# Performance work log

Hardware: AMD Instinct MI355X
Metric: run time of the kernel (lower is better)

Reference implementation:

```python
import jax, jax.numpy as jnp
import numpy as np
from jax import lax

B, T, HW = 8, 32, 128
D, NH, DEPTH, DFF = 384, 6, 6, 1536
PR = PC = 4
P = PR * PC
EPS = 1e-5


def _ln(x, g, b):
    mu = x.mean(-1, keepdims=True)
    v = ((x - mu) ** 2).mean(-1, keepdims=True)
    return (x - mu) / jnp.sqrt(v + EPS) * g + b


def _conv2d(x, w, s, p):
    return lax.conv_general_dilated(x, w, (s, s), [(p, p), (p, p)],
                                    dimension_numbers=('NCHW', 'OIHW', 'NCHW'))


def _bn(x, g, b, m, v):
    inv = g / jnp.sqrt(v + EPS)
    return x * inv[:, None, None] + (b - m * inv)[:, None, None]


def _gelu(x):
    return jax.nn.gelu(x, approximate=False)


def _forward(frames, conv1_w, bn1_g, bn1_b, bn1_m, bn1_v,
             conv2_w, bn2_g, bn2_b, bn2_m, bn2_v,
             conv3_w, bn3_g, bn3_b, bn3_m, bn3_v, proj_w,
             dw_w, dw_b, pw_w, pw_b, tnorm_g, tnorm_b,
             frame_pos, patch_pos, cls_token, cls_pos,
             qkv_w, qkv_b, out_w, out_b, ln1_g, ln1_b, ln2_g, ln2_b,
             ffn_w1, ffn_b1, ffn_w2, ffn_b2,
             head_ln_g, head_ln_b, head_w1, head_b1, head_w2, head_b2):
    b, t = frames.shape[0], frames.shape[1]
    # ---- FrameEncoder (eval-mode BN) ----
    x = frames.reshape(b * t, 1, HW, HW)
    x = _gelu(_bn(_conv2d(x, conv1_w, 2, 2), bn1_g, bn1_b, bn1_m, bn1_v))
    x = _gelu(_bn(_conv2d(x, conv2_w, 2, 1), bn2_g, bn2_b, bn2_m, bn2_v))
    x = _gelu(_bn(_conv2d(x, conv3_w, 2, 1), bn3_g, bn3_b, bn3_m, bn3_v))
    n, c, hh, ww = x.shape
    # adaptive avg pool (16,16)->(4,4) is an exact 4x4 mean pool
    x = x.reshape(n, c, PR, hh // PR, PC, ww // PC).mean(axis=(3, 5))
    x = jnp.einsum('oc,nchw->nohw', proj_w[:, :, 0, 0], x)  # 1x1 conv proj
    tokens = x.reshape(n, D, P).transpose(0, 2, 1).reshape(b, t, P, D)
    # ---- TemporalConvBlock (per-patch sequences) ----
    tc = tokens.transpose(0, 2, 1, 3).reshape(b * P, t, D)
    out = tc.transpose(0, 2, 1)  # [N, D, t]
    for i, dil in enumerate((1, 2)):
        pad = dil * (3 - 1) // 2
        h = lax.conv_general_dilated(out, dw_w[i], (1,), [(pad, pad)],
                                     rhs_dilation=(dil,), feature_group_count=D,
                                     dimension_numbers=('NCH', 'OIH', 'NCH'))
        h = _gelu(h + dw_b[i][None, :, None])
        h = jnp.einsum('oi,nit->not', pw_w[i], h) + pw_b[i][None, :, None]
        out = h + out
    out = out.transpose(0, 2, 1)
    tc = _ln(out + tc, tnorm_g, tnorm_b)
    tokens = tc.reshape(b, P, t, D).transpose(0, 2, 1, 3)
    # ---- positional + cls ----
    fp = frame_pos[:t].transpose(1, 0, 2)[:, :, None, :]  # [1,t,1,D]
    pp = patch_pos[:, None, :, :]                          # [1,1,P,D]
    tok = (tokens + fp + pp).reshape(b, t * P, D)
    cls = cls_token + cls_pos
    tok = jnp.concatenate([jnp.broadcast_to(cls, (b, 1, D)), tok], axis=1)
    S = t * P + 1
    # ---- block-structured additive mask (faithful to _build_causal_mask) ----
    ids = jnp.repeat(jnp.arange(t), P)
    neg = jnp.finfo(jnp.float32).min
    base = jnp.where(ids[None, :] < ids[:, None], neg, 0.0)
    mask = jnp.zeros((S, S), jnp.float32).at[1:, 1:].set(base).at[1:, 0].set(neg)
    # ---- pre-norm transformer encoder ----
    hd = D // NH
    scale = 1.0 / jnp.sqrt(jnp.float32(hd))
    x = tok
    for i in range(DEPTH):
        h = _ln(x, ln1_g[i], ln1_b[i])
        qkv = h @ qkv_w[i].T + qkv_b[i]
        q, k, v = jnp.split(qkv, 3, axis=-1)
        q = q.reshape(b, S, NH, hd).transpose(0, 2, 1, 3)
        k = k.reshape(b, S, NH, hd).transpose(0, 2, 1, 3)
        v = v.reshape(b, S, NH, hd).transpose(0, 2, 1, 3)
        scores = jnp.einsum('bhqd,bhkd->bhqk', q, k) * scale + mask
        a = jax.nn.softmax(scores, axis=-1)
        o = jnp.einsum('bhqk,bhkd->bhqd', a, v).transpose(0, 2, 1, 3).reshape(b, S, D)
        x = x + (o @ out_w[i].T + out_b[i])
        h2 = _ln(x, ln2_g[i], ln2_b[i])
        x = x + _gelu(h2 @ ffn_w1[i].T + ffn_b1[i]) @ ffn_w2[i].T + ffn_b2[i]
    # ---- coord head ----
    pooled = x[:, 0]
    h = _ln(pooled, head_ln_g, head_ln_b)
    h = _gelu(h @ head_w1.T + head_b1)
    coords = jax.nn.sigmoid(h @ head_w2.T + head_b2)
    return coords


def setup_inputs():
    ks = iter(jax.random.split(jax.random.key(0), 64))

    def r(shape, s):
        return jax.random.normal(next(ks), shape, jnp.float32) * s

    inp = {}
    inp['frames'] = jax.random.normal(next(ks), (B, T, 1, HW, HW), jnp.float32)
    inp['conv1_w'] = r((32, 1, 5, 5), 0.2)
    inp['bn1_g'] = jnp.ones(32); inp['bn1_b'] = jnp.zeros(32)
    inp['bn1_m'] = r((32,), 0.1)
    inp['bn1_v'] = jax.random.uniform(next(ks), (32,), jnp.float32, 0.5, 1.5)
    inp['conv2_w'] = r((64, 32, 3, 3), 0.1)
    inp['bn2_g'] = jnp.ones(64); inp['bn2_b'] = jnp.zeros(64)
    inp['bn2_m'] = r((64,), 0.1)
    inp['bn2_v'] = jax.random.uniform(next(ks), (64,), jnp.float32, 0.5, 1.5)
    inp['conv3_w'] = r((128, 64, 3, 3), 0.07)
    inp['bn3_g'] = jnp.ones(128); inp['bn3_b'] = jnp.zeros(128)
    inp['bn3_m'] = r((128,), 0.1)
    inp['bn3_v'] = jax.random.uniform(next(ks), (128,), jnp.float32, 0.5, 1.5)
    inp['proj_w'] = r((D, 128, 1, 1), 0.08)
    inp['dw_w'] = r((2, D, 1, 3), 0.3)
    inp['dw_b'] = jnp.zeros((2, D))
    inp['pw_w'] = r((2, D, D), 0.05)
    inp['pw_b'] = jnp.zeros((2, D))
    inp['tnorm_g'] = jnp.ones(D); inp['tnorm_b'] = jnp.zeros(D)
    inp['frame_pos'] = r((T, 1, D), 0.02)
    inp['patch_pos'] = r((1, P, D), 0.02)
    inp['cls_token'] = jnp.zeros((1, 1, D))
    inp['cls_pos'] = r((1, 1, D), 0.02)
    inp['qkv_w'] = r((DEPTH, 3 * D, D), 0.02)
    inp['qkv_b'] = jnp.zeros((DEPTH, 3 * D))
    inp['out_w'] = r((DEPTH, D, D), 0.02)
    inp['out_b'] = jnp.zeros((DEPTH, D))
    inp['ln1_g'] = jnp.ones((DEPTH, D)); inp['ln1_b'] = jnp.zeros((DEPTH, D))
    inp['ln2_g'] = jnp.ones((DEPTH, D)); inp['ln2_b'] = jnp.zeros((DEPTH, D))
    inp['ffn_w1'] = r((DEPTH, DFF, D), 0.02)
    inp['ffn_b1'] = jnp.zeros((DEPTH, DFF))
    inp['ffn_w2'] = r((DEPTH, D, DFF), 0.02)
    inp['ffn_b2'] = jnp.zeros((DEPTH, D))
    inp['head_ln_g'] = jnp.ones(D); inp['head_ln_b'] = jnp.zeros(D)
    inp['head_w1'] = r((D, D), 0.02); inp['head_b1'] = jnp.zeros(D)
    inp['head_w2'] = r((2, D), 0.02); inp['head_b2'] = jnp.zeros(2)
    return inp


def reference(frames, conv1_w, bn1_g, bn1_b, bn1_m, bn1_v,
              conv2_w, bn2_g, bn2_b, bn2_m, bn2_v,
              conv3_w, bn3_g, bn3_b, bn3_m, bn3_v, proj_w,
              dw_w, dw_b, pw_w, pw_b, tnorm_g, tnorm_b,
              frame_pos, patch_pos, cls_token, cls_pos,
              qkv_w, qkv_b, out_w, out_b, ln1_g, ln1_b, ln2_g, ln2_b,
              ffn_w1, ffn_b1, ffn_w2, ffn_b2,
              head_ln_g, head_ln_b, head_w1, head_b1, head_w2, head_b2):
    return _forward(frames, conv1_w, bn1_g, bn1_b, bn1_m, bn1_v,
                    conv2_w, bn2_g, bn2_b, bn2_m, bn2_v,
                    conv3_w, bn3_g, bn3_b, bn3_m, bn3_v, proj_w,
                    dw_w, dw_b, pw_w, pw_b, tnorm_g, tnorm_b,
                    frame_pos, patch_pos, cls_token, cls_pos,
                    qkv_w, qkv_b, out_w, out_b, ln1_g, ln1_b, ln2_g, ln2_b,
                    ffn_w1, ffn_b1, ffn_w2, ffn_b2,
                    head_ln_g, head_ln_b, head_w1, head_b1, head_w2, head_b2)
```

## Files before the change

### kernel.cpp

```cpp
#include <hip/hip_runtime.h>
#include <hip/hip_fp16.h>
#include <cstddef>

#define EPSV 1e-5f

typedef _Float16 f16;
typedef _Float16 f16x8 __attribute__((ext_vector_type(8)));
typedef float f32x4v __attribute__((ext_vector_type(4)));

__device__ __forceinline__ float gelu_f(float x) {
    return 0.5f * x * (1.0f + erff(x * 0.7071067811865476f));
}

__device__ __forceinline__ float gelu_fast(float x) {
    float y = 0.7978845608f * (x + 0.044715f * x * x * x);
    y = fminf(fmaxf(y, -10.f), 10.f);
    float e = __expf(2.f * y);
    float t = (e - 1.f) / (e + 1.f);
    return 0.5f * x * (1.f + t);
}

__global__ __launch_bounds__(256) void cvt_all_kernel(
    const float* __restrict__ p0, const float* __restrict__ p1,
    const float* __restrict__ p2, const float* __restrict__ p3,
    const float* __restrict__ p4, const float* __restrict__ p5,
    f16* __restrict__ dst)
{
    const int n = 10960896;
    for (int i = blockIdx.x * 256 + threadIdx.x; i < n; i += gridDim.x * 256) {
        const float* s; int off;
        if      (i <   49152) { s = p0; off = i; }
        else if (i <  344064) { s = p1; off = i -   49152; }
        else if (i < 2998272) { s = p2; off = i -  344064; }
        else if (i < 3883008) { s = p3; off = i - 2998272; }
        else if (i < 7421952) { s = p4; off = i - 3883008; }
        else                  { s = p5; off = i - 7421952; }
        dst[i] = (f16)s[off];
    }
}

__global__ __launch_bounds__(256) void conv_w_reorder_kernel(
    const float* __restrict__ w, f16* __restrict__ out, int CO, int CI)
{
    int n = CO * CI * 9;
    for (int i = blockIdx.x * 256 + threadIdx.x; i < n; i += gridDim.x * 256) {
        int t = i % 9; int r = i / 9;
        int ci = r % CI; int co = r / CI;
        out[(size_t)co * CI * 9 + t * CI + ci] = (f16)w[i];
    }
}

__global__ __launch_bounds__(256) void conv1_wave_kernel(
    const float* __restrict__ in, const float* __restrict__ w,
    const float* __restrict__ g, const float* __restrict__ bt,
    const float* __restrict__ mn, const float* __restrict__ vr,
    f16* __restrict__ out)
{
    __shared__ float inp[35][37];
    int bid = blockIdx.x;
    int n = bid >> 4; int tile = bid & 15;
    int ty0 = (tile >> 2) * 16, tx0 = (tile & 3) * 16;
    int t = threadIdx.x;
    const float* ip = in + (size_t)n * 16384;
    for (int e = t; e < 35 * 36; e += 256) {
        int r = e / 36, c = e - r * 36;
        int iy = ty0 * 2 - 2 + r, ix = tx0 * 2 - 2 + c;
        inp[r][c] = ((unsigned)iy < 128u && (unsigned)ix < 128u) ? ip[iy * 128 + ix] : 0.f;
    }
    __syncthreads();
    int wv = __builtin_amdgcn_readfirstlane(t >> 6);
    int lane = t & 63;
    int cobase = wv * 8;
    float sc[8], be[8];
    #pragma unroll
    for (int c = 0; c < 8; c++) {
        int co = cobase + c;
        float iv = g[co] * rsqrtf(vr[co] + EPSV);
        sc[c] = iv; be[c] = bt[co] - mn[co] * iv;
    }
    #pragma unroll
    for (int pix = 0; pix < 4; pix++) {
        int p = pix * 64 + lane;
        int py = p >> 4, px = p & 15;
        float r0[25];
        #pragma unroll
        for (int ky = 0; ky < 5; ky++)
            #pragma unroll
            for (int kx = 0; kx < 5; kx++)
                r0[ky * 5 + kx] = inp[2 * py + ky][2 * px + kx];
        f16 o[8];
        #pragma unroll
        for (int c = 0; c < 8; c++) {
            const float* wp = w + (cobase + c) * 25;
            float acc = 0.f;
            #pragma unroll
            for (int k = 0; k < 25; k++) acc += wp[k] * r0[k];
            o[c] = (f16)gelu_fast(acc * sc[c] + be[c]);
        }
        size_t ob = (((size_t)n * 64 + ty0 + py) * 64 + tx0 + px) * 32 + cobase;
        *(uint4*)(out + ob) = *(uint4*)o;
    }
}

template<int CI, int HI, int CO>
__global__ __launch_bounds__(256) void convg_kernel(
    const f16* __restrict__ in, const f16* __restrict__ wr_,
    const float* __restrict__ g, const float* __restrict__ bt,
    const float* __restrict__ mn, const float* __restrict__ vr,
    f16* __restrict__ out)
{
    constexpr int HO = HI / 2;
    constexpr int HOB = (HO == 32) ? 5 : 4;
    constexpr int K = 9 * CI;
    __shared__ __align__(16) f16 As[64 * 40];
    __shared__ __align__(16) f16 Bs[64 * 40];
    int tid = threadIdx.x;
    int bm = blockIdx.x * 64;
    int bn = blockIdx.y * 64;
    int lrow = tid >> 2, lseg = tid & 3;
    int w = tid >> 6, lane = tid & 63;
    int wr = (w >> 1) * 32, wc = (w & 1) * 32;
    int l15 = lane & 15, l4 = lane >> 4;
    int gp = bm + lrow;
    int pn = gp >> (2 * HOB);
    int prem = gp & ((1 << (2 * HOB)) - 1);
    int oy = prem >> HOB, ox = prem & (HO - 1);

    f32x4v zero = {0.f, 0.f, 0.f, 0.f};
    f32x4v acc[2][2];
    acc[0][0] = zero; acc[0][1] = zero; acc[1][0] = zero; acc[1][1] = zero;

    auto loadTile = [&](int k0, uint4& av, uint4& bv) {
        int tap = k0 / CI;
        int cio = k0 - tap * CI;
        int ky = tap / 3, kx = tap - ky * 3;
        int iy = oy * 2 - 1 + ky, ix = ox * 2 - 1 + kx;
        av = make_uint4(0u, 0u, 0u, 0u);
        if ((unsigned)iy < (unsigned)HI && (unsigned)ix < (unsigned)HI)
            av = *(const uint4*)(in + (((size_t)(pn * HI + iy)) * HI + ix) * CI + cio + lseg * 8);
        bv = *(const uint4*)(wr_ + (size_t)(bn + lrow) * K + k0 + lseg * 8);
    };

    uint4 ra, rb;
    loadTile(0, ra, rb);
    for (int k0 = 0; k0 < K; k0 += 32) {
        __syncthreads();
        *(uint4*)(&As[lrow * 40 + lseg * 8]) = ra;
        *(uint4*)(&Bs[lrow * 40 + lseg * 8]) = rb;
        if (k0 + 32 < K) loadTile(k0 + 32, ra, rb);
        __syncthreads();
        f16x8 a0 = *(const f16x8*)(&As[(wr + l15) * 40 + l4 * 8]);
        f16x8 a1 = *(const f16x8*)(&As[(wr + 16 + l15) * 40 + l4 * 8]);
        f16x8 b0 = *(const f16x8*)(&Bs[(wc + l15) * 40 + l4 * 8]);
        f16x8 b1 = *(const f16x8*)(&Bs[(wc + 16 + l15) * 40 + l4 * 8]);
        acc[0][0] = __builtin_amdgcn_mfma_f32_16x16x32_f16(a0, b0, acc[0][0], 0, 0, 0);
        acc[0][1] = __builtin_amdgcn_mfma_f32_16x16x32_f16(a0, b1, acc[0][1], 0, 0, 0);
        acc[1][0] = __builtin_amdgcn_mfma_f32_16x16x32_f16(a1, b0, acc[1][0], 0, 0, 0);
        acc[1][1] = __builtin_amdgcn_mfma_f32_16x16x32_f16(a1, b1, acc[1][1], 0, 0, 0);
    }
    float inv[2], beta[2];
    #pragma unroll
    for (int ni = 0; ni < 2; ni++) {
        int col = bn + wc + ni * 16 + l15;
        float iv = g[col] * rsqrtf(vr[col] + EPSV);
        inv[ni] = iv; beta[ni] = bt[col] - mn[col] * iv;
    }
    #pragma unroll
    for (int mi = 0; mi < 2; mi++) {
        #pragma unroll
        for (int q = 0; q < 4; q++) {
            int pixel = bm + wr + mi * 16 + l4 * 4 + q;
            #pragma unroll
            for (int ni = 0; ni < 2; ni++) {
                int col = bn + wc + ni * 16 + l15;
                float v = acc[mi][ni][q] * inv[ni] + beta[ni];
                out[(size_t)pixel * CO + col] = (f16)gelu_fast(v);
            }
        }
    }
}

__global__ __launch_bounds__(256) void poolh_kernel(
    const f16* __restrict__ in, f16* __restrict__ out, int NC)
{
    int idx = blockIdx.x * 256 + threadIdx.x;
    if (idx >= NC * 16 * 16) return;
    int cc = idx & 15; int npl = idx >> 4;
    int c0 = cc * 8;
    int n = npl >> 4; int p = npl & 15;
    int ph = p >> 2, pw = p & 3;
    const f16* base = in + (((size_t)(n * 16 + ph * 4)) * 16 + pw * 4) * 128 + c0;
    float s[8] = {};
    #pragma unroll
    for (int dy = 0; dy < 4; dy++)
        #pragma unroll
        for (int dx = 0; dx < 4; dx++) {
            f16x8 v = *(const f16x8*)(base + (dy * 16 + dx) * 128);
            #pragma unroll
            for (int u = 0; u < 8; u++) s[u] += (float)v[u];
        }
    f16* op = out + (size_t)npl * 128 + c0;
    #pragma unroll
    for (int u = 0; u < 8; u++) op[u] = (f16)(s[u] * 0.0625f);
}

template<int OUTF16, int ACT, int VTRANS>
__global__ __launch_bounds__(256) void gemm_k64_kernel(
    const f16* __restrict__ A, const f16* __restrict__ B,
    const float* __restrict__ bias, const float* __restrict__ res,
    void* __restrict__ Cv, f16* __restrict__ vT, int M, int N, int K, int nrow)
{
    __shared__ __align__(16) f16 As[64 * 72];
    __shared__ __align__(16) f16 Bs[64 * 72];
    int nb = gridDim.x;
    int q = nb >> 3, r = nb & 7;
    int xcd = blockIdx.x & 7, pos = blockIdx.x >> 3;
    int logical = (xcd < r ? xcd * (q + 1) : r * (q + 1) + (xcd - r) * q) + pos;
    int brow = logical % nrow, bcol = logical / nrow;
    int bm = brow * 64, bn = bcol * 64;

    int tid = threadIdx.x;
    int lrow = tid >> 2, lseg = (tid & 3) * 16;
    int w = tid >> 6, lane = tid & 63;
    int wr = (w >> 1) * 32, wc = (w & 1) * 32;
    int l15 = lane & 15, l4 = lane >> 4;
    f32x4v zero = {0.f, 0.f, 0.f, 0.f};
    f32x4v acc[2][2];
    acc[0][0] = zero; acc[0][1] = zero; acc[1][0] = zero; acc[1][1] = zero;

    int arow = bm + lrow;
    bool aok = (arow < M);
    const f16* ap = A + (size_t)arow * K + lseg;
    const f16* bp = B + (size_t)(bn + lrow) * K + lseg;

    uint4 ra0 = make_uint4(0u,0u,0u,0u), ra1 = ra0, rb0, rb1;
    if (aok) { ra0 = *(const uint4*)(ap); ra1 = *(const uint4*)(ap + 8); }
    rb0 = *(const uint4*)(bp); rb1 = *(const uint4*)(bp + 8);

    int nt = K >> 6;
    for (int t = 0; t < nt; t++) {
        __syncthreads();
        *(uint4*)(&As[lrow * 72 + lseg])     = ra0;
        *(uint4*)(&As[lrow * 72 + lseg + 8]) = ra1;
        *(uint4*)(&Bs[lrow * 72 + lseg])     = rb0;
        *(uint4*)(&Bs[lrow * 72 + lseg + 8]) = rb1;
        if (t + 1 < nt) {
            int k0 = (t + 1) << 6;
            if (aok) { ra0 = *(const uint4*)(ap + k0); ra1 = *(const uint4*)(ap + k0 + 8); }
            rb0 = *(const uint4*)(bp + k0); rb1 = *(const uint4*)(bp + k0 + 8);
        }
        __syncthreads();
        #pragma unroll
        for (int s = 0; s < 2; s++) {
            f16x8 a0 = *(const f16x8*)(&As[(wr + l15) * 72 + s * 32 + l4 * 8]);
            f16x8 a1 = *(const f16x8*)(&As[(wr + 16 + l15) * 72 + s * 32 + l4 * 8]);
            f16x8 b0 = *(const f16x8*)(&Bs[(wc + l15) * 72 + s * 32 + l4 * 8]);
            f16x8 b1 = *(const f16x8*)(&Bs[(wc + 16 + l15) * 72 + s * 32 + l4 * 8]);
            acc[0][0] = __builtin_amdgcn_mfma_f32_16x16x32_f16(a0, b0, acc[0][0], 0, 0, 0);
            acc[0][1] = __builtin_amdgcn_mfma_f32_16x16x32_f16(a0, b1, acc[0][1], 0, 0, 0);
            acc[1][0] = __builtin_amdgcn_mfma_f32_16x16x32_f16(a1, b0, acc[1][0], 0, 0, 0);
            acc[1][1] = __builtin_amdgcn_mfma_f32_16x16x32_f16(a1, b1, acc[1][1], 0, 0, 0);
        }
    }

    if (VTRANS && bn >= 768) {
        __syncthreads();
        f16* tile = As;
        #pragma unroll
        for (int mi = 0; mi < 2; mi++)
            #pragma unroll
            for (int qq = 0; qq < 4; qq++) {
                int rl = wr + mi * 16 + l4 * 4 + qq;
                #pragma unroll
                for (int ni = 0; ni < 2; ni++) {
                    int dl = wc + ni * 16 + l15;
                    float v = acc[mi][ni][qq] + bias[bn + dl];
                    tile[dl * 66 + rl] = (f16)v;
                }
            }
        __syncthreads();
        int h = (bn - 768) >> 6;
        int j = tid & 63, dbase = tid >> 6;
        int trow = bm + j;
        if (trow < M) {
            int b = trow / 513;
            int jj = trow - b * 513;
            f16* vb = vT + ((size_t)(b * 6 + h) * 64) * 576 + jj;
            #pragma unroll
            for (int it = 0; it < 16; it++) {
                int d = dbase * 16 + it;
                vb[(size_t)d * 576] = tile[d * 66 + j];
            }
        }
        return;
    }
    #pragma unroll
    for (int mi = 0; mi < 2; mi++) {
        #pragma unroll
        for (int qq = 0; qq < 4; qq++) {
            int row = bm + wr + mi * 16 + l4 * 4 + qq;
            if (row >= M) continue;
            #pragma unroll
            for (int ni = 0; ni < 2; ni++) {
                int col = bn + wc + ni * 16 + l15;
                float v = acc[mi][ni][qq];
                if (bias) v += bias[col];
                if (ACT == 1) v = gelu_fast(v);
                if (res) v += res[(size_t)row * N + col];
                if (OUTF16) ((f16*)Cv)[(size_t)row * N + col] = (f16)v;
                else ((float*)Cv)[(size_t)row * N + col] = v;
            }
        }
    }
}

__global__ __launch_bounds__(256) void tok2tc_kernel(
    const float* __restrict__ in, float* __restrict__ out)
{
    int idx = blockIdx.x * 256 + threadIdx.x;
    if (idx >= 8 * 32 * 16 * 384) return;
    int d = idx % 384; int t2 = idx / 384;
    int p = t2 & 15; t2 >>= 4;
    int t = t2 & 31; int b = t2 >> 5;
    out[(((size_t)(b * 16 + p) * 32 + t) * 384) + d] = in[idx];
}

__global__ __launch_bounds__(256) void dwconv_kernel(
    const float* __restrict__ in, const float* __restrict__ w,
    const float* __restrict__ bias, f16* __restrict__ out, int dil)
{
    int idx = blockIdx.x * 256 + threadIdx.x;
    if (idx >= 128 * 32 * 384) return;
    int d = idx % 384; int t = (idx / 384) & 31; int s = idx / (384 * 32);
    const float* ip = in + (size_t)s * 32 * 384 + d;
    float acc = bias[d];
    #pragma unroll
    for (int k = 0; k < 3; k++) {
        int tt = t + (k - 1) * dil;
        if ((unsigned)tt < 32u) acc += w[d * 3 + k] * ip[tt * 384];
    }
    out[idx] = (f16)gelu_fast(acc);
}

__global__ __launch_bounds__(256) void ln_wave_kernel(
    const float* __restrict__ in,
    const float* __restrict__ g, const float* __restrict__ b,
    f16* __restrict__ out, int rows)
{
    int w = threadIdx.x >> 6, lane = threadIdx.x & 63;
    int row = blockIdx.x * 4 + w;
    if (row >= rows) return;
    const float* ip = in + (size_t)row * 384;
    float x[6]; float s = 0.f, s2 = 0.f;
    #pragma unroll
    for (int k = 0; k < 6; k++) {
        float v = ip[lane + 64 * k];
        x[k] = v; s += v; s2 += v * v;
    }
    #pragma unroll
    for (int off = 1; off < 64; off <<= 1) {
        s += __shfl_xor(s, off); s2 += __shfl_xor(s2, off);
    }
    float mu = s * (1.f / 384.f);
    float var = s2 * (1.f / 384.f) - mu * mu;
    float rs = rsqrtf(var + EPSV);
    #pragma unroll
    for (int k = 0; k < 6; k++) {
        int c = lane + 64 * k;
        out[(size_t)row * 384 + c] = (f16)((x[k] - mu) * rs * g[c] + b[c]);
    }
}

__global__ __launch_bounds__(128) void build_x_kernel(
    const float* __restrict__ mix, const float* __restrict__ tc,
    const float* __restrict__ tg, const float* __restrict__ tb,
    const float* __restrict__ fpos, const float* __restrict__ ppos,
    float* __restrict__ x)
{
    int row = blockIdx.x;
    int t = row & 31; int bp = row >> 5;
    int p = bp & 15; int b = bp >> 4;
    int tid = threadIdx.x;
    const float* ip = mix + (size_t)row * 384;
    const float* ip2 = tc + (size_t)row * 384;
    __shared__ float red[128], red2[128];
    float v[3]; float s = 0.f, s2 = 0.f;
    #pragma unroll
    for (int j = 0; j < 3; j++) {
        float val = ip[tid + 128 * j] + ip2[tid + 128 * j];
        v[j] = val; s += val; s2 += val * val;
    }
    red[tid] = s; red2[tid] = s2; __syncthreads();
    for (int off = 64; off >= 1; off >>= 1) {
        if (tid < off) { red[tid] += red[tid + off]; red2[tid] += red2[tid + off]; }
        __syncthreads();
    }
    float mu = red[0] * (1.f / 384.f);
    float var = red2[0] * (1.f / 384.f) - mu * mu;
    float rs = rsqrtf(var + EPSV);
    size_t xbase = ((size_t)b * 513 + 1 + t * 16 + p) * 384;
    #pragma unroll
    for (int j = 0; j < 3; j++) {
        int c = tid + 128 * j;
        float y = (v[j] - mu) * rs * tg[c] + tb[c] + fpos[t * 384 + c] + ppos[p * 384 + c];
        x[xbase + c] = y;
    }
}

__global__ __launch_bounds__(256) void cls_kernel(
    const float* __restrict__ ct, const float* __restrict__ cp, float* __restrict__ x)
{
    int idx = blockIdx.x * 256 + threadIdx.x;
    if (idx >= 8 * 384) return;
    int c = idx % 384; int b = idx / 384;
    x[(size_t)b * 513 * 384 + c] = ct[c] + cp[c];
}

__global__ __launch_bounds__(256) void fattn_split_kernel(
    const f16* __restrict__ qkv, const f16* __restrict__ vT,
    float* __restrict__ Op, float* __restrict__ ml)
{
    __shared__ __align__(16) f16 Pl[4][16][72];
    int qt = blockIdx.x;
    int bh = blockIdx.y; int h = bh % 6; int b = bh / 6;
    int third = blockIdx.z;
    int tid = threadIdx.x;
    int w = tid >> 6, lane = tid & 63;
    int l15 = lane & 15, g = lane >> 4;
    int q0w = qt * 64 + w * 16;
    if (q0w > 512) return;
    const size_t RS = 1152;
    const f16* qbase = qkv + (size_t)b * 513 * RS + h * 64;
    const f16* kbase = qbase + 384;
    const f16* vtb = vT + (size_t)bh * 64 * 576;

    f16x8 qf[2];
    {
        int qrow = q0w + l15; if (qrow > 512) qrow = 512;
        const f16* qp = qbase + (size_t)qrow * RS + g * 8;
        qf[0] = *(const f16x8*)(qp);
        qf[1] = *(const f16x8*)(qp + 32);
    }

    f32x4v zero = {0.f, 0.f, 0.f, 0.f};
    f32x4v O[4]; float m[4], l[4];
    #pragma unroll
    for (int i = 0; i < 4; i++) { O[i] = zero; m[i] = -INFINITY; l[i] = 0.f; }

    int jt0 = 0;
    if (q0w > 0) { int fmin = (q0w - 1) >> 4; jt0 = (fmin * 16 + 1) >> 6; }

    int jrow[4];
    #pragma unroll
    for (int jf = 0; jf < 4; jf++) jrow[jf] = jf * 16 + l15;

    auto loadK = [&](int j0, f16x8* kr) {
        #pragma unroll
        for (int s = 0; s < 2; s++)
            #pragma unroll
            for (int jf = 0; jf < 4; jf++) {
                int j = j0 + jrow[jf]; if (j > 512) j = 512;
                kr[s * 4 + jf] = *(const f16x8*)(kbase + (size_t)j * RS + s * 32 + g * 8);
            }
    };

    int jt = jt0 + third;
    f16x8 kreg[8];
    if (jt < 9) loadK(jt * 64, kreg);

    for (; jt < 9; jt += 3) {
        int j0 = jt * 64;
        f16x8 vreg[8];
        #pragma unroll
        for (int s = 0; s < 2; s++)
            #pragma unroll
            for (int df = 0; df < 4; df++)
                vreg[s * 4 + df] = *(const f16x8*)(vtb + (size_t)(df * 16 + l15) * 576 + j0 + s * 32 + g * 8);
        f32x4v S[4];
        #pragma unroll
        for (int jf = 0; jf < 4; jf++) S[jf] = zero;
        #pragma unroll
        for (int s = 0; s < 2; s++)
            #pragma unroll
            for (int jf = 0; jf < 4; jf++)
                S[jf] = __builtin_amdgcn_mfma_f32_16x16x32_f16(qf[s], kreg[s * 4 + jf], S[jf], 0, 0, 0);
        f16x8 knext[8];
        if (jt + 3 < 9) loadK((jt + 3) * 64, knext);
        float pj[4][4];
        #pragma unroll
        for (int r = 0; r < 4; r++) {
            int qi = q0w + 4 * g + r;
            int fi = (qi == 0) ? -1 : ((qi - 1) >> 4);
            float mx = -INFINITY;
            #pragma unroll
            for (int jf = 0; jf < 4; jf++) {
                int j = j0 + jrow[jf];
                bool valid = (qi < 513) && (j < 513) &&
                             !((qi != 0) && ((j == 0) || (((j - 1) >> 4) < fi)));
                float sv = valid ? S[jf][r] * 0.125f : -INFINITY;
                pj[jf][r] = sv;
                mx = fmaxf(mx, sv);
            }
            mx = fmaxf(mx, __shfl_xor(mx, 1));
            mx = fmaxf(mx, __shfl_xor(mx, 2));
            mx = fmaxf(mx, __shfl_xor(mx, 4));
            mx = fmaxf(mx, __shfl_xor(mx, 8));
            float mn = fmaxf(m[r], mx);
            float alpha = (m[r] == -INFINITY) ? 0.f : __expf(m[r] - mn);
            float ls = 0.f;
            #pragma unroll
            for (int jf = 0; jf < 4; jf++) {
                float p = (pj[jf][r] == -INFINITY) ? 0.f : __expf(pj[jf][r] - mn);
                pj[jf][r] = p; ls += p;
            }
            ls += __shfl_xor(ls, 1); ls += __shfl_xor(ls, 2);
            ls += __shfl_xor(ls, 4); ls += __shfl_xor(ls, 8);
            l[r] = alpha * l[r] + ls;
            m[r] = mn;
            #pragma unroll
            for (int df = 0; df < 4; df++) O[df][r] *= alpha;
        }
        #pragma unroll
        for (int jf = 0; jf < 4; jf++)
            #pragma unroll
            for (int r = 0; r < 4; r++)
                Pl[w][4 * g + r][jf * 16 + l15] = (f16)pj[jf][r];
        #pragma unroll
        for (int s = 0; s < 2; s++) {
            f16x8 pf = *(const f16x8*)(&Pl[w][l15][s * 32 + g * 8]);
            #pragma unroll
            for (int df = 0; df < 4; df++)
                O[df] = __builtin_amdgcn_mfma_f32_16x16x32_f16(pf, vreg[s * 4 + df], O[df], 0, 0, 0);
        }
        #pragma unroll
        for (int i = 0; i < 8; i++) kreg[i] = knext[i];
    }

    int rowbase = third * 24624 + bh * 513;
    #pragma unroll
    for (int r = 0; r < 4; r++) {
        int qi = q0w + 4 * g + r;
        if (qi > 512) continue;
        size_t ro = (size_t)(rowbase + qi);
        #pragma unroll
        for (int df = 0; df < 4; df++)
            Op[ro * 64 + df * 16 + l15] = O[df][r];
        if (l15 == 0) {
            ml[ro * 2 + 0] = m[r];
            ml[ro * 2 + 1] = l[r];
        }
    }
}

__global__ __launch_bounds__(256) void attn_combine_kernel(
    const float* __restrict__ Op, const float* __restrict__ ml,
    f16* __restrict__ ob)
{
    int row = blockIdx.x * 4 + (threadIdx.x >> 6);
    if (row >= 24624) return;
    int lane = threadIdx.x & 63;
    int bh = row / 513, qi = row - bh * 513;
    int b = bh / 6, h = bh - b * 6;
    float mv[3], lv[3], mm = -INFINITY;
    #pragma unroll
    for (int s = 0; s < 3; s++) {
        mv[s] = ml[((size_t)s * 24624 + row) * 2];
        lv[s] = ml[((size_t)s * 24624 + row) * 2 + 1];
        mm = fmaxf(mm, mv[s]);
    }
    float onum = 0.f, lden = 0.f;
    #pragma unroll
    for (int s = 0; s < 3; s++) {
        float a = (mv[s] == -INFINITY) ? 0.f : __expf(mv[s] - mm);
        lden += lv[s] * a;
        onum += Op[((size_t)s * 24624 + row) * 64 + lane] * a;
    }
    ob[((size_t)(b * 513 + qi)) * 384 + h * 64 + lane] = (f16)(onum / lden);
}

__global__ __launch_bounds__(384) void head_kernel(
    const float* __restrict__ x, const float* __restrict__ lg, const float* __restrict__ lb,
    const float* __restrict__ w1, const float* __restrict__ b1,
    const float* __restrict__ w2, const float* __restrict__ b2,
    float* __restrict__ out)
{
    int b = blockIdx.x; int t = threadIdx.x;
    __shared__ float hs[384], h1[384];
    __shared__ float rs[6], rs2[6];
    const float* xp = x + (size_t)b * 513 * 384;
    float v = xp[t];
    float s = v, s2 = v * v;
    #pragma unroll
    for (int off = 32; off >= 1; off >>= 1) {
        s += __shfl_down(s, off); s2 += __shfl_down(s2, off);
    }
    if ((t & 63) == 0) { rs[t >> 6] = s; rs2[t >> 6] = s2; }
    __syncthreads();
    float S = 0.f, S2 = 0.f;
    #pragma unroll
    for (int i = 0; i < 6; i++) { S += rs[i]; S2 += rs2[i]; }
    float mu = S * (1.f / 384.f);
    float var = S2 * (1.f / 384.f) - mu * mu;
    float rstd = rsqrtf(var + EPSV);
    hs[t] = (v - mu) * rstd * lg[t] + lb[t];
    __syncthreads();
    const float* wr = w1 + (size_t)t * 384;
    float acc = b1[t];
    for (int c = 0; c < 384; c += 4) {
        float4 w4 = *reinterpret_cast<const float4*>(wr + c);
        acc += w4.x * hs[c] + w4.y * hs[c + 1] + w4.z * hs[c + 2] + w4.w * hs[c + 3];
    }
    h1[t] = gelu_f(acc);
    __syncthreads();
    float p0 = h1[t] * w2[t], p1 = h1[t] * w2[384 + t];
    #pragma unroll
    for (int off = 32; off >= 1; off >>= 1) {
        p0 += __shfl_down(p0, off); p1 += __shfl_down(p1, off);
    }
    if ((t & 63) == 0) { rs[t >> 6] = p0; rs2[t >> 6] = p1; }
    __syncthreads();
    if (t == 0) {
        float a0 = b2[0], a1 = b2[1];
        #pragma unroll
        for (int i = 0; i < 6; i++) { a0 += rs[i]; a1 += rs2[i]; }
        out[b * 2 + 0] = 1.f / (1.f + expf(-a0));
        out[b * 2 + 1] = 1.f / (1.f + expf(-a1));
    }
}

static inline int cdiv(int a, int b) { return (a + b - 1) / b; }

extern "C" void kernel_launch(void* const* d_in, const int* in_sizes, int n_in,
                              void* d_out, int out_size, void* d_ws, size_t ws_size,
                              hipStream_t stream)
{
    const float* frames  = (const float*)d_in[0];
    const float* conv1_w = (const float*)d_in[1];
    const float* bn1_g = (const float*)d_in[2]; const float* bn1_b = (const float*)d_in[3];
    const float* bn1_m = (const float*)d_in[4]; const float* bn1_v = (const float*)d_in[5];
    const float* conv2_w = (const float*)d_in[6];
    const float* bn2_g = (const float*)d_in[7]; const float* bn2_b = (const float*)d_in[8];
    const float* bn2_m = (const float*)d_in[9]; const float* bn2_v = (const float*)d_in[10];
    const float* conv3_w = (const float*)d_in[11];
    const float* bn3_g = (const float*)d_in[12]; const float* bn3_b = (const float*)d_in[13];
    const float* bn3_m = (const float*)d_in[14]; const float* bn3_v = (const float*)d_in[15];
    const float* proj_w = (const float*)d_in[16];
    const float* dw_w = (const float*)d_in[17]; const float* dw_b = (const float*)d_in[18];
    const float* pw_w = (const float*)d_in[19]; const float* pw_b = (const float*)d_in[20];
    const float* tnorm_g = (const float*)d_in[21]; const float* tnorm_b = (const float*)d_in[22];
    const float* frame_pos = (const float*)d_in[23];
    const float* patch_pos = (const float*)d_in[24];
    const float* cls_token = (const float*)d_in[25];
    const float* cls_pos = (const float*)d_in[26];
    const float* qkv_w = (const float*)d_in[27]; const float* qkv_b = (const float*)d_in[28];
    const float* out_w = (const float*)d_in[29]; const float* out_b = (const float*)d_in[30];
    const float* ln1_g = (const float*)d_in[31]; const float* ln1_b = (const float*)d_in[32];
    const float* ln2_g = (const float*)d_in[33]; const float* ln2_b = (const float*)d_in[34];
    const float* ffn_w1 = (const float*)d_in[35]; const float* ffn_b1 = (const float*)d_in[36];
    const float* ffn_w2 = (const float*)d_in[37]; const float* ffn_b2 = (const float*)d_in[38];
    const float* head_ln_g = (const float*)d_in[39]; const float* head_ln_b = (const float*)d_in[40];
    const float* head_w1 = (const float*)d_in[41]; const float* head_b1 = (const float*)d_in[42];
    const float* head_w2 = (const float*)d_in[43]; const float* head_b2 = (const float*)d_in[44];
    (void)in_sizes; (void)n_in; (void)out_size; (void)ws_size;

    char* base = (char*)d_ws;
    size_t off = 0;
    auto alloc = [&](size_t bytes) { void* p = base + off; off = (off + bytes + 255) & ~(size_t)255; return p; };

    f16* wtotal = (f16*)alloc((size_t)10960896 * 2);
    f16* projw16 = wtotal;
    f16* pw16    = wtotal + 49152;
    f16* qkvw16  = wtotal + 344064;
    f16* outw16  = wtotal + 2998272;
    f16* f1w16   = wtotal + 3883008;
    f16* f2w16   = wtotal + 7421952;
    f16* c2w16   = (f16*)alloc((size_t)64 * 288 * 2);
    f16* c3w16   = (f16*)alloc((size_t)128 * 576 * 2);
    float* tokens = (float*)alloc((size_t)4096 * 384 * 4);
    f16* pooled   = (f16*)alloc((size_t)4096 * 128 * 2);

    size_t ustart = off;
    f16* c1h = (f16*)alloc((size_t)256 * 64 * 64 * 32 * 2);
    f16* c2h = (f16*)alloc((size_t)256 * 32 * 32 * 64 * 2);
    f16* c3h = (f16*)alloc((size_t)256 * 16 * 16 * 128 * 2);
    size_t uend_stem = off;
    off = ustart;
    float* tc = (float*)alloc((size_t)4096 * 384 * 4);
    float* mA = (float*)alloc((size_t)4096 * 384 * 4);
    float* mB = (float*)alloc((size_t)4096 * 384 * 4);
    f16*   mh = (f16*)alloc((size_t)4096 * 384 * 2);
    float* xb   = (float*)alloc((size_t)8 * 513 * 384 * 4);
    f16*   hb   = (f16*)alloc((size_t)8 * 513 * 384 * 2);
    f16*   qkvb = (f16*)alloc((size_t)8 * 513 * 1152 * 2);
    f16*   vTb  = (f16*)alloc((size_t)48 * 64 * 576 * 2);
    f16*   ob   = (f16*)alloc((size_t)8 * 513 * 384 * 2);
    f16*   ffb  = (f16*)alloc((size_t)8 * 513 * 1536 * 2);
    float* Opart = (float*)alloc((size_t)3 * 24624 * 64 * 4);
    float* mlpart = (float*)alloc((size_t)3 * 24624 * 2 * 4);
    if (off < uend_stem) off = uend_stem;

    cvt_all_kernel<<<4096, 256, 0, stream>>>(
        proj_w, pw_w, qkv_w, out_w, ffn_w1, ffn_w2, wtotal);
    conv_w_reorder_kernel<<<cdiv(64 * 288, 256), 256, 0, stream>>>(conv2_w, c2w16, 64, 32);
    conv_w_reorder_kernel<<<cdiv(128 * 576, 256), 256, 0, stream>>>(conv3_w, c3w16, 128, 64);

    conv1_wave_kernel<<<256 * 16, 256, 0, stream>>>(
        frames, conv1_w, bn1_g, bn1_b, bn1_m, bn1_v, c1h);
    convg_kernel<32, 64, 64><<<dim3(4096, 1), 256, 0, stream>>>(
        c1h, c2w16, bn2_g, bn2_b, bn2_m, bn2_v, c2h);
    convg_kernel<64, 32, 128><<<dim3(1024, 2), 256, 0, stream>>>(
        c2h, c3w16, bn3_g, bn3_b, bn3_m, bn3_v, c3h);
    poolh_kernel<<<256, 256, 0, stream>>>(c3h, pooled, 256);
    gemm_k64_kernel<0, 0, 0><<<384, 256, 0, stream>>>(
        pooled, projw16, nullptr, nullptr, tokens, nullptr, 4096, 384, 128, 64);

    tok2tc_kernel<<<cdiv(8 * 32 * 16 * 384, 256), 256, 0, stream>>>(tokens, tc);
    dwconv_kernel<<<cdiv(128 * 32 * 384, 256), 256, 0, stream>>>(
        tc, dw_w, dw_b, mh, 1);
    gemm_k64_kernel<0, 0, 0><<<384, 256, 0, stream>>>(
        mh, pw16, pw_b, tc, mA, nullptr, 4096, 384, 384, 64);
    dwconv_kernel<<<cdiv(128 * 32 * 384, 256), 256, 0, stream>>>(
        mA, dw_w + 384 * 3, dw_b + 384, mh, 2);
    gemm_k64_kernel<0, 0, 0><<<384, 256, 0, stream>>>(
        mh, pw16 + 384 * 384, pw_b + 384, mA, mB, nullptr, 4096, 384, 384, 64);

    build_x_kernel<<<128 * 32, 128, 0, stream>>>(
        mB, tc, tnorm_g, tnorm_b, frame_pos, patch_pos, xb);
    cls_kernel<<<cdiv(8 * 384, 256), 256, 0, stream>>>(cls_token, cls_pos, xb);

    const int M = 8 * 513;
    const int NR = cdiv(M, 64);
    for (int l = 0; l < 6; l++) {
        ln_wave_kernel<<<cdiv(M, 4), 256, 0, stream>>>(xb,
            ln1_g + (size_t)l * 384, ln1_b + (size_t)l * 384, hb, M);
        gemm_k64_kernel<1, 0, 1><<<NR * 18, 256, 0, stream>>>(
            hb, qkvw16 + (size_t)l * 1152 * 384, qkv_b + (size_t)l * 1152,
            nullptr, qkvb, vTb, M, 1152, 384, NR);
        fattn_split_kernel<<<dim3(9, 48, 3), 256, 0, stream>>>(qkvb, vTb, Opart, mlpart);
        attn_combine_kernel<<<cdiv(24624, 4), 256, 0, stream>>>(Opart, mlpart, ob);
        gemm_k64_kernel<0, 0, 0><<<NR * 6, 256, 0, stream>>>(
            ob, outw16 + (size_t)l * 384 * 384, out_b + (size_t)l * 384,
            xb, xb, nullptr, M, 384, 384, NR);
        ln_wave_kernel<<<cdiv(M, 4), 256, 0, stream>>>(xb,
            ln2_g + (size_t)l * 384, ln2_b + (size_t)l * 384, hb, M);
        gemm_k64_kernel<1, 1, 0><<<NR * 24, 256, 0, stream>>>(
            hb, f1w16 + (size_t)l * 1536 * 384, ffn_b1 + (size_t)l * 1536,
            nullptr, ffb, nullptr, M, 1536, 384, NR);
        gemm_k64_kernel<0, 0, 0><<<NR * 6, 256, 0, stream>>>(
            ffb, f2w16 + (size_t)l * 384 * 1536, ffn_b2 + (size_t)l * 384,
            xb, xb, nullptr, M, 384, 1536, NR);
    }

    head_kernel<<<8, 384, 0, stream>>>(
        xb, head_ln_g, head_ln_b, head_w1, head_b1, head_w2, head_b2, (float*)d_out);
}
```

Measured before the change: 869.6 us.

## Use MFMA for conv1, wider-N tile for FFN1 GEMM, fp16 attention partials

Conv1 now runs as a small MFMA GEMM. It uses fp16 input patches in shared memory and BN-scaled fp16 weights prepared by a new prep kernel, replacing the scalar fp32 FMA loop. The FFN1 GEMM gets a dedicated 64x128 tile kernel with an XCD-aware block remap, which halves the block count and raises per-block reuse of the A tile. Split-attention partial outputs are stored as fp16 instead of fp32 to cut the memory traffic between the attention and combine kernels. The costs are reduced precision in conv1 inputs and in the attention partials, and less parallelism in FFN1.

```diff
diff --git a/kernel.cpp b/kernel.cpp
--- a/kernel.cpp
+++ b/kernel.cpp
@@ -50,13 +50,25 @@
     }
 }
 
-__global__ __launch_bounds__(256) void conv1_wave_kernel(
-    const float* __restrict__ in, const float* __restrict__ w,
-    const float* __restrict__ g, const float* __restrict__ bt,
-    const float* __restrict__ mn, const float* __restrict__ vr,
+__global__ __launch_bounds__(256) void conv1_w_prep_kernel(
+    const float* __restrict__ w, const float* __restrict__ g,
+    const float* __restrict__ vr, f16* __restrict__ wB)
+{
+    int i = blockIdx.x * 256 + threadIdx.x;
+    if (i >= 1024) return;
+    int co = i >> 5, k = i & 31;
+    float inv = g[co] * rsqrtf(vr[co] + EPSV);
+    wB[i] = (f16)((k < 25) ? w[co * 25 + k] * inv : 0.f);
+}
+
+__global__ __launch_bounds__(256) void conv1_mfma_kernel(
+    const float* __restrict__ in, const f16* __restrict__ wB,
+    const float* __restrict__ bt, const float* __restrict__ mn,
+    const float* __restrict__ g, const float* __restrict__ vr,
     f16* __restrict__ out)
 {
-    __shared__ float inp[35][37];
+    __shared__ __align__(16) f16 inpH[35 * 36 + 8];
+    __shared__ __align__(16) f16 Bs[32 * 32];
     int bid = blockIdx.x;
     int n = bid >> 4; int tile = bid & 15;
     int ty0 = (tile >> 2) * 16, tx0 = (tile & 3) * 16;
@@ -65,40 +77,61 @@
     for (int e = t; e < 35 * 36; e += 256) {
         int r = e / 36, c = e - r * 36;
         int iy = ty0 * 2 - 2 + r, ix = tx0 * 2 - 2 + c;
-        inp[r][c] = ((unsigned)iy < 128u && (unsigned)ix < 128u) ? ip[iy * 128 + ix] : 0.f;
+        float v = ((unsigned)iy < 128u && (unsigned)ix < 128u && c < 35) ? ip[iy * 128 + ix] : 0.f;
+        inpH[e] = (f16)v;
+    }
+    if (t < 128) {
+        int row = t >> 2, seg = (t & 3) * 8;
+        *(uint4*)(&Bs[row * 32 + seg]) = *(const uint4*)(wB + row * 32 + seg);
     }
     __syncthreads();
-    int wv = __builtin_amdgcn_readfirstlane(t >> 6);
-    int lane = t & 63;
-    int cobase = wv * 8;
-    float sc[8], be[8];
-    #pragma unroll
-    for (int c = 0; c < 8; c++) {
-        int co = cobase + c;
-        float iv = g[co] * rsqrtf(vr[co] + EPSV);
-        sc[c] = iv; be[c] = bt[co] - mn[co] * iv;
-    }
-    #pragma unroll
-    for (int pix = 0; pix < 4; pix++) {
-        int p = pix * 64 + lane;
-        int py = p >> 4, px = p & 15;
-        float r0[25];
-        #pragma unroll
-        for (int ky = 0; ky < 5; ky++)
-            #pragma unroll
-            for (int kx = 0; kx < 5; kx++)
-                r0[ky * 5 + kx] = inp[2 * py + ky][2 * px + kx];
-        f16 o[8];
-        #pragma unroll
-        for (int c = 0; c < 8; c++) {
-            const float* wp = w + (cobase + c) * 25;
-            float acc = 0.f;
-            #pragma unroll
-            for (int k = 0; k < 25; k++) acc += wp[k] * r0[k];
-            o[c] = (f16)gelu_fast(acc * sc[c] + be[c]);
-        }
-        size_t ob = (((size_t)n * 64 + ty0 + py) * 64 + tx0 + px) * 32 + cobase;
-        *(uint4*)(out + ob) = *(uint4*)o;
+    int w = t >> 6, lane = t & 63;
+    int l15 = lane & 15, gq = lane >> 4;
+    f16x8 afr[4];
+    #pragma unroll
+    for (int i = 0; i < 4; i++) {
+        int mt = 4 * w + i;
+        f16 tmp[8];
+        #pragma unroll
+        for (int e = 0; e < 8; e++) {
+            int kk = 8 * gq + e; if (kk > 24) kk = 24;
+            int ky = kk / 5, kx = kk - ky * 5;
+            tmp[e] = inpH[(2 * mt + ky) * 36 + 2 * l15 + kx];
+        }
+        afr[i] = *(f16x8*)tmp;
+    }
+    f16x8 bfr[2];
+    bfr[0] = *(const f16x8*)(&Bs[l15 * 32 + 8 * gq]);
+    bfr[1] = *(const f16x8*)(&Bs[(16 + l15) * 32 + 8 * gq]);
+    f32x4v zero = {0.f, 0.f, 0.f, 0.f};
+    f32x4v acc[4][2];
+    #pragma unroll
+    for (int i = 0; i < 4; i++) { acc[i][0] = zero; acc[i][1] = zero; }
+    #pragma unroll
+    for (int i = 0; i < 4; i++) {
+        acc[i][0] = __builtin_amdgcn_mfma_f32_16x16x32_f16(afr[i], bfr[0], acc[i][0], 0, 0, 0);
+        acc[i][1] = __builtin_amdgcn_mfma_f32_16x16x32_f16(afr[i], bfr[1], acc[i][1], 0, 0, 0);
+    }
+    float beta[2];
+    #pragma unroll
+    for (int nt = 0; nt < 2; nt++) {
+        int co = nt * 16 + l15;
+        float inv = g[co] * rsqrtf(vr[co] + EPSV);
+        beta[nt] = bt[co] - mn[co] * inv;
+    }
+    #pragma unroll
+    for (int i = 0; i < 4; i++) {
+        int y = ty0 + 4 * w + i;
+        #pragma unroll
+        for (int q = 0; q < 4; q++) {
+            int x = tx0 + 4 * gq + q;
+            size_t ob = (((size_t)n * 64 + y) * 64 + x) * 32;
+            #pragma unroll
+            for (int nt = 0; nt < 2; nt++) {
+                int co = nt * 16 + l15;
+                out[ob + co] = (f16)gelu_fast(acc[i][nt][q] + beta[nt]);
+            }
+        }
     }
 }
 
@@ -314,6 +347,92 @@
     }
 }
 
+template<int ACT>
+__global__ __launch_bounds__(256) void gemm_kn128_kernel(
+    const f16* __restrict__ A, const f16* __restrict__ B,
+    const float* __restrict__ bias, f16* __restrict__ C,
+    int M, int N, int K, int nrow)
+{
+    __shared__ __align__(16) f16 As[64 * 72];
+    __shared__ __align__(16) f16 Bs[128 * 72];
+    int nb = gridDim.x;
+    int q = nb >> 3, r = nb & 7;
+    int xcd = blockIdx.x & 7, pos = blockIdx.x >> 3;
+    int logical = (xcd < r ? xcd * (q + 1) : r * (q + 1) + (xcd - r) * q) + pos;
+    int brow = logical % nrow, bcol = logical / nrow;
+    int bm = brow * 64, bn = bcol * 128;
+
+    int tid = threadIdx.x;
+    int w = tid >> 6, lane = tid & 63;
+    int wr = (w >> 1) * 32, wc = (w & 1) * 64;
+    int l15 = lane & 15, l4 = lane >> 4;
+    int alrow = tid >> 2, alseg = (tid & 3) * 16;
+    int blrow = tid >> 1, blseg = (tid & 1) * 32;
+
+    f32x4v zero = {0.f, 0.f, 0.f, 0.f};
+    f32x4v acc[2][4];
+    #pragma unroll
+    for (int i = 0; i < 2; i++)
+        #pragma unroll
+        for (int j = 0; j < 4; j++) acc[i][j] = zero;
+
+    int arow = bm + alrow;
+    bool aok = (arow < M);
+    const f16* ap = A + (size_t)arow * K + alseg;
+    const f16* bp = B + (size_t)(bn + blrow) * K + blseg;
+
+    uint4 ra0 = make_uint4(0u,0u,0u,0u), ra1 = ra0;
+    uint4 rb0, rb1, rb2, rb3;
+    if (aok) { ra0 = *(const uint4*)(ap); ra1 = *(const uint4*)(ap + 8); }
+    rb0 = *(const uint4*)(bp);      rb1 = *(const uint4*)(bp + 8);
+    rb2 = *(const uint4*)(bp + 16); rb3 = *(const uint4*)(bp + 24);
+
+    int ntiles = K >> 6;
+    for (int t = 0; t < ntiles; t++) {
+        __syncthreads();
+        *(uint4*)(&As[alrow * 72 + alseg])     = ra0;
+        *(uint4*)(&As[alrow * 72 + alseg + 8]) = ra1;
+        *(uint4*)(&Bs[blrow * 72 + blseg])      = rb0;
+        *(uint4*)(&Bs[blrow * 72 + blseg + 8])  = rb1;
+        *(uint4*)(&Bs[blrow * 72 + blseg + 16]) = rb2;
+        *(uint4*)(&Bs[blrow * 72 + blseg + 24]) = rb3;
+        if (t + 1 < ntiles) {
+            int k0 = (t + 1) << 6;
+            if (aok) { ra0 = *(const uint4*)(ap + k0); ra1 = *(const uint4*)(ap + k0 + 8); }
+            rb0 = *(const uint4*)(bp + k0);      rb1 = *(const uint4*)(bp + k0 + 8);
+            rb2 = *(const uint4*)(bp + k0 + 16); rb3 = *(const uint4*)(bp + k0 + 24);
+        }
+        __syncthreads();
+        #pragma unroll
+        for (int s = 0; s < 2; s++) {
+            f16x8 a0 = *(const f16x8*)(&As[(wr + l15) * 72 + s * 32 + l4 * 8]);
+            f16x8 a1 = *(const f16x8*)(&As[(wr + 16 + l15) * 72 + s * 32 + l4 * 8]);
+            #pragma unroll
+            for (int j = 0; j < 4; j++) {
+                f16x8 bf = *(const f16x8*)(&Bs[(wc + j * 16 + l15) * 72 + s * 32 + l4 * 8]);
+                acc[0][j] = __builtin_amdgcn_mfma_f32_16x16x32_f16(a0, bf, acc[0][j], 0, 0, 0);
+                acc[1][j] = __builtin_amdgcn_mfma_f32_16x16x32_f16(a1, bf, acc[1][j], 0, 0, 0);
+            }
+        }
+    }
+    #pragma unroll
+    for (int mi = 0; mi < 2; mi++) {
+        #pragma unroll
+        for (int qq = 0; qq < 4; qq++) {
+            int row = bm + wr + mi * 16 + l4 * 4 + qq;
+            if (row >= M) continue;
+            #pragma unroll
+            for (int j = 0; j < 4; j++) {
+                int col = bn + wc + j * 16 + l15;
+                float v = acc[mi][j][qq];
+                if (bias) v += bias[col];
+                if (ACT == 1) v = gelu_fast(v);
+                C[(size_t)row * N + col] = (f16)v;
+            }
+        }
+    }
+}
+
 __global__ __launch_bounds__(256) void tok2tc_kernel(
     const float* __restrict__ in, float* __restrict__ out)
 {
@@ -418,7 +537,7 @@
 
 __global__ __launch_bounds__(256) void fattn_split_kernel(
     const f16* __restrict__ qkv, const f16* __restrict__ vT,
-    float* __restrict__ Op, float* __restrict__ ml)
+    f16* __restrict__ Op, float* __restrict__ ml)
 {
     __shared__ __align__(16) f16 Pl[4][16][72];
     int qt = blockIdx.x;
@@ -544,7 +663,7 @@
         size_t ro = (size_t)(rowbase + qi);
         #pragma unroll
         for (int df = 0; df < 4; df++)
-            Op[ro * 64 + df * 16 + l15] = O[df][r];
+            Op[ro * 64 + df * 16 + l15] = (f16)O[df][r];
         if (l15 == 0) {
             ml[ro * 2 + 0] = m[r];
             ml[ro * 2 + 1] = l[r];
@@ -553,7 +672,7 @@
 }
 
 __global__ __launch_bounds__(256) void attn_combine_kernel(
-    const float* __restrict__ Op, const float* __restrict__ ml,
+    const f16* __restrict__ Op, const float* __restrict__ ml,
     f16* __restrict__ ob)
 {
     int row = blockIdx.x * 4 + (threadIdx.x >> 6);
@@ -573,7 +692,7 @@
     for (int s = 0; s < 3; s++) {
         float a = (mv[s] == -INFINITY) ? 0.f : __expf(mv[s] - mm);
         lden += lv[s] * a;
-        onum += Op[((size_t)s * 24624 + row) * 64 + lane] * a;
+        onum += (float)Op[((size_t)s * 24624 + row) * 64 + lane] * a;
     }
     ob[((size_t)(b * 513 + qi)) * 384 + h * 64 + lane] = (f16)(onum / lden);
 }
@@ -674,6 +793,7 @@
     f16* outw16  = wtotal + 2998272;
     f16* f1w16   = wtotal + 3883008;
     f16* f2w16   = wtotal + 7421952;
+    f16* c1wB    = (f16*)alloc(1024 * 2);
     f16* c2w16   = (f16*)alloc((size_t)64 * 288 * 2);
     f16* c3w16   = (f16*)alloc((size_t)128 * 576 * 2);
     float* tokens = (float*)alloc((size_t)4096 * 384 * 4);
@@ -695,17 +815,18 @@
     f16*   vTb  = (f16*)alloc((size_t)48 * 64 * 576 * 2);
     f16*   ob   = (f16*)alloc((size_t)8 * 513 * 384 * 2);
     f16*   ffb  = (f16*)alloc((size_t)8 * 513 * 1536 * 2);
-    float* Opart = (float*)alloc((size_t)3 * 24624 * 64 * 4);
+    f16*   Opart = (f16*)alloc((size_t)3 * 24624 * 64 * 2);
     float* mlpart = (float*)alloc((size_t)3 * 24624 * 2 * 4);
     if (off < uend_stem) off = uend_stem;
 
     cvt_all_kernel<<<4096, 256, 0, stream>>>(
         proj_w, pw_w, qkv_w, out_w, ffn_w1, ffn_w2, wtotal);
+    conv1_w_prep_kernel<<<4, 256, 0, stream>>>(conv1_w, bn1_g, bn1_v, c1wB);
     conv_w_reorder_kernel<<<cdiv(64 * 288, 256), 256, 0, stream>>>(conv2_w, c2w16, 64, 32);
     conv_w_reorder_kernel<<<cdiv(128 * 576, 256), 256, 0, stream>>>(conv3_w, c3w16, 128, 64);
 
-    conv1_wave_kernel<<<256 * 16, 256, 0, stream>>>(
-        frames, conv1_w, bn1_g, bn1_b, bn1_m, bn1_v, c1h);
+    conv1_mfma_kernel<<<256 * 16, 256, 0, stream>>>(
+        frames, c1wB, bn1_b, bn1_m, bn1_g, bn1_v, c1h);
     convg_kernel<32, 64, 64><<<dim3(4096, 1), 256, 0, stream>>>(
         c1h, c2w16, bn2_g, bn2_b, bn2_m, bn2_v, c2h);
     convg_kernel<64, 32, 128><<<dim3(1024, 2), 256, 0, stream>>>(
@@ -743,9 +864,9 @@
             xb, xb, nullptr, M, 384, 384, NR);
         ln_wave_kernel<<<cdiv(M, 4), 256, 0, stream>>>(xb,
             ln2_g + (size_t)l * 384, ln2_b + (size_t)l * 384, hb, M);
-        gemm_k64_kernel<1, 1, 0><<<NR * 24, 256, 0, stream>>>(
+        gemm_kn128_kernel<1><<<NR * 12, 256, 0, stream>>>(
             hb, f1w16 + (size_t)l * 1536 * 384, ffn_b1 + (size_t)l * 1536,
-            nullptr, ffb, nullptr, M, 1536, 384, NR);
+            ffb, M, 1536, 384, NR);
         gemm_k64_kernel<0, 0, 0><<<NR * 6, 256, 0, stream>>>(
             ffb, f2w16 + (size_t)l * 384 * 1536, ffn_b2 + (size_t)l * 384,
             xb, xb, nullptr, M, 384, 1536, NR);
```

Measured after the change: 851.0 us. 2.1% less time.
